# Kernel optimization log

Hardware: AMD Instinct MI355X
Metric: run time of the kernel (lower is better)

## Reference

```python
import jax, jax.numpy as jnp
import numpy as np

B, C, OUT, H, W, M1, M2, HID = 4, 64, 64, 256, 256, 32, 32, 64
COORD = C + 1  # MLP input: channels + 1 coordinate


def _lin(key, fan_in, fan_out):
    lim = 1.0 / np.sqrt(fan_in)
    kw, kb = jax.random.split(key)
    Wm = jax.random.uniform(kw, (fan_in, fan_out), minval=-lim, maxval=lim, dtype=jnp.float32)
    b = jax.random.uniform(kb, (fan_out,), minval=-lim, maxval=lim, dtype=jnp.float32)
    return Wm, b


def setup_inputs() -> dict:
    key = jax.random.key(0)
    ks = jax.random.split(key, 12)
    x = jax.random.normal(ks[0], (B, C, H, W), dtype=jnp.float32)
    # basis_w MLP: (C+1) -> HID -> HID -> 2*M2
    wW0, wb0 = _lin(ks[1], COORD, HID)
    wW1, wb1 = _lin(ks[2], HID, HID)
    wW2, wb2 = _lin(ks[3], HID, 2 * M2)
    # basis_h MLP: (C+1) -> HID -> HID -> 2*M1
    hW0, hb0 = _lin(ks[4], COORD, HID)
    hW1, hb1 = _lin(ks[5], HID, HID)
    hW2, hb2 = _lin(ks[6], HID, 2 * M1)
    std = (1.0 / (C + OUT)) ** 0.5
    Wf_re = std * jax.random.normal(ks[7], (C, OUT, M1, M2), dtype=jnp.float32)
    Wf_im = std * jax.random.normal(ks[8], (C, OUT, M1, M2), dtype=jnp.float32)
    mixer_w, mixer_b = _lin(ks[9], OUT, OUT)
    mixer_w = mixer_w.T  # (out, in) conv1x1 layout
    sc_w, sc_b = _lin(ks[10], C, OUT)
    sc_w = sc_w.T
    return {
        "x": x,
        "wW0": wW0, "wb0": wb0, "wW1": wW1, "wb1": wb1, "wW2": wW2, "wb2": wb2,
        "hW0": hW0, "hb0": hb0, "hW1": hW1, "hb1": hb1, "hW2": hW2, "hb2": hb2,
        "Wf_re": Wf_re, "Wf_im": Wf_im,
        "mixer_w": mixer_w, "mixer_b": mixer_b,
        "sc_w": sc_w, "sc_b": sc_b,
    }


def _gelu(v):
    return jax.nn.gelu(v, approximate=False)  # torch GELU is exact erf


def _cmlp(x, W0, b0, W1, b1, W2, b2, m):
    h = _gelu(x @ W0 + b0)
    h = _gelu(h @ W1 + b1)
    o = h @ W2 + b2
    return jax.lax.complex(o[..., :m], o[..., m:])


def reference(x, wW0, wb0, wW1, wb1, wW2, wb2,
              hW0, hb0, hW1, hb1, hW2, hb2,
              Wf_re, Wf_im, mixer_w, mixer_b, sc_w, sc_b):
    Bb, Cc, Hh, Ww = x.shape
    # --- W-direction basis: input is (values, w-coord) per pixel ---
    wc = jnp.linspace(-1.0, 1.0, Ww, dtype=jnp.float32)
    w_in = jnp.concatenate(
        [jnp.transpose(x, (0, 2, 3, 1)),
         jnp.broadcast_to(wc[None, None, :, None], (Bb, Hh, Ww, 1))], axis=-1)
    wb = _cmlp(w_in, wW0, wb0, wW1, wb1, wW2, wb2, M2)  # (B,H,W,m2) complex
    xc = x.astype(jnp.complex64)
    # separable transform along W: contract W against runtime basis
    tfw = jnp.einsum('bchw,bhwm->bchm', xc, wb)  # (B,C,H,m2)
    # --- H-direction basis: input is real part of W-transform + h-coord ---
    hcv = jnp.linspace(-1.0, 1.0, Hh, dtype=jnp.float32)
    h_in = jnp.concatenate(
        [jnp.transpose(tfw.real, (0, 3, 2, 1)),
         jnp.broadcast_to(hcv[None, None, :, None], (Bb, M2, Hh, 1))], axis=-1)
    hb = _cmlp(h_in, hW0, hb0, hW1, hb1, hW2, hb2, M1)  # (B,m2,H,m1) complex
    tfhw = jnp.einsum('bchm,bmhk->bckm', tfw, hb)  # (B,C,m1,m2)
    Wf = jax.lax.complex(Wf_re, Wf_im)  # (C_in, C_out, m1, m2)
    proc = jnp.einsum('bixy,oixy->boxy', tfhw, Wf)  # (B,out,m1,m2)
    # inverse transforms with conjugate-transposed bases
    rec = jnp.einsum('bokm,bmhk->bohm', proc, jnp.conj(hb))  # (B,out,H,m2)
    spatial = jnp.einsum('bohm,bhwm->bohw', rec, jnp.conj(wb)).real / (Hh * Ww)
    y = jnp.einsum('bchw,oc->bohw', spatial, mixer_w) + mixer_b[None, :, None, None]
    y = _gelu(y)
    y = y + jnp.einsum('bchw,oc->bohw', x, sc_w) + sc_b[None, :, None, None]
    return _gelu(y)
```

## Files before the change

### kernel.cpp

```cpp
#include <hip/hip_runtime.h>
#include <math.h>


typedef __attribute__((ext_vector_type(8))) short bf16x8;
typedef __attribute__((ext_vector_type(4))) float f32x4;

__device__ __forceinline__ float gelu_f(float v) {
    return 0.5f * v * (1.0f + erff(v * 0.70710678118654752440f));
}

__device__ __forceinline__ unsigned short f2b(float f) {
    union { float f; unsigned int u; } v; v.f = f;
    unsigned int u = v.u + 0x7FFFu + ((v.u >> 16) & 1u);
    return (unsigned short)(u >> 16);
}
__device__ __forceinline__ float b2f(unsigned short b) {
    union { unsigned int u; float f; } v; v.u = ((unsigned int)b) << 16;
    return v.f;
}

__global__ void k_prep(const float* __restrict__ wW0, const float* __restrict__ wW1,
                       const float* __restrict__ wW2,
                       const float* __restrict__ hW0, const float* __restrict__ hW1,
                       const float* __restrict__ hW2,
                       unsigned short* __restrict__ wT0, unsigned short* __restrict__ wT1,
                       unsigned short* __restrict__ wT2,
                       unsigned short* __restrict__ hT0, unsigned short* __restrict__ hT1,
                       unsigned short* __restrict__ hT2)
{
    const int t = threadIdx.x;
    for (int idx = t; idx < 64 * 96; idx += 256) {
        const int o = idx / 96, k = idx % 96;
        wT0[idx] = (k < 65) ? f2b(wW0[k * 64 + o]) : (unsigned short)0;
        hT0[idx] = (k < 65) ? f2b(hW0[k * 64 + o]) : (unsigned short)0;
    }
    for (int idx = t; idx < 4096; idx += 256) {
        const int o = idx >> 6, k = idx & 63;
        wT1[idx] = f2b(wW1[k * 64 + o]);
        wT2[idx] = f2b(wW2[k * 64 + o]);
        hT1[idx] = f2b(hW1[k * 64 + o]);
        hT2[idx] = f2b(hW2[k * 64 + o]);
    }
}

__global__ __launch_bounds__(256) void k_psum(const float* __restrict__ src,
                                              float* __restrict__ dst,
                                              int nparts, int part_stride)
{
    const int i = (blockIdx.x * 256 + threadIdx.x) * 4;
    float4 acc = *(const float4*)&src[i];
    for (int p = 1; p < nparts; ++p) {
        const float4 v = *(const float4*)&src[(size_t)p * part_stride + i];
        acc.x += v.x; acc.y += v.y; acc.z += v.z; acc.w += v.w;
    }
    *(float4*)&dst[i] = acc;
}

__global__ __launch_bounds__(256) void k_psum_procT(const float* __restrict__ src,
                                                    float* __restrict__ dst)
{
    const int idx = blockIdx.x * 256 + threadIdx.x;
    const int o = idx & 63, k = (idx >> 6) & 31, m = (idx >> 11) & 31, b = idx >> 16;
    const size_t in = (size_t)(b * 64 + o) * 1024 + k * 32 + m;
    const float re = src[in] + src[524288 + in];
    const float im = src[262144 + in] + src[524288 + 262144 + in];
    dst[idx] = re;
    dst[262144 + idx] = im;
}

constexpr int MLD = 104;

template<bool GELU, int NKC>
__device__ __forceinline__ void mfma_layer(
    const unsigned short* __restrict__ sW,
    const unsigned short* __restrict__ sAct,
    unsigned short* __restrict__ dst,
    const float* __restrict__ bias, int lane, int wv)
{
    const int arow = lane & 15;
    const int koff = (lane >> 4) * 8;
    const int crow = 16 * wv + (lane >> 4) * 4;
    const f32x4 zero = {0.f, 0.f, 0.f, 0.f};
    f32x4 acc[4] = {zero, zero, zero, zero};
#pragma unroll
    for (int kc = 0; kc < NKC; ++kc) {
        const bf16x8 a = *(const bf16x8*)&sW[(16 * wv + arow) * MLD + kc * 32 + koff];
#pragma unroll
        for (int nt = 0; nt < 4; ++nt) {
            const bf16x8 b = *(const bf16x8*)&sAct[(nt * 16 + arow) * MLD + kc * 32 + koff];
            acc[nt] = __builtin_amdgcn_mfma_f32_16x16x32_bf16(a, b, acc[nt], 0, 0, 0);
        }
    }
    const float4 bv = *(const float4*)&bias[crow];
#pragma unroll
    for (int nt = 0; nt < 4; ++nt) {
        const int px = nt * 16 + arow;
        float v0 = acc[nt][0] + bv.x;
        float v1 = acc[nt][1] + bv.y;
        float v2 = acc[nt][2] + bv.z;
        float v3 = acc[nt][3] + bv.w;
        if (GELU) { v0 = gelu_f(v0); v1 = gelu_f(v1); v2 = gelu_f(v2); v3 = gelu_f(v3); }
        ushort4 u;
        u.x = f2b(v0); u.y = f2b(v1); u.z = f2b(v2); u.w = f2b(v3);
        *(ushort4*)&dst[px * MLD + crow] = u;
    }
}

__device__ __forceinline__ void stage_wT96(const unsigned short* __restrict__ src,
                                           unsigned short* __restrict__ sW, int t) {
#pragma unroll
    for (int r = 0; r < 3; ++r) {
        const int idx = r * 256 + t;
        const int row = idx / 12, f = idx % 12;
        *(uint4*)&sW[row * MLD + f * 8] = *(const uint4*)&src[row * 96 + f * 8];
    }
}
__device__ __forceinline__ void stage_wT64(const unsigned short* __restrict__ src,
                                           unsigned short* __restrict__ sW, int t) {
#pragma unroll
    for (int r = 0; r < 2; ++r) {
        const int idx = r * 256 + t;
        const int row = idx >> 3, f = idx & 7;
        *(uint4*)&sW[row * MLD + f * 8] = *(const uint4*)&src[row * 64 + f * 8];
    }
}

__global__ __launch_bounds__(256) void k_wb_mlp2(
    const float* __restrict__ x,
    const unsigned short* __restrict__ wT0, const float* __restrict__ b0,
    const unsigned short* __restrict__ wT1, const float* __restrict__ b1,
    const unsigned short* __restrict__ wT2, const float* __restrict__ b2,
    unsigned short* __restrict__ wb_bf, unsigned short* __restrict__ wbT)
{
    __shared__ __align__(16) unsigned short sA[64 * MLD];
    __shared__ __align__(16) unsigned short sB[64 * MLD];
    __shared__ __align__(16) unsigned short sW[64 * MLD];
    const int blk = blockIdx.x;
    const int b = blk >> 10, h = (blk >> 2) & 255, wq = blk & 3;
    const int w0 = wq * 64;
    const int t = threadIdx.x;
    const int lane = t & 63, wv = t >> 6;

#pragma unroll
    for (int r = 0; r < 4; ++r) {
        const int idx = r * 256 + t;
        const int c = idx >> 4, wg = idx & 15;
        const float4 v = *(const float4*)&x[((size_t)(b * 64 + c) * 256 + h) * 256 + w0 + wg * 4];
        sA[(wg * 4 + 0) * MLD + c] = f2b(v.x);
        sA[(wg * 4 + 1) * MLD + c] = f2b(v.y);
        sA[(wg * 4 + 2) * MLD + c] = f2b(v.z);
        sA[(wg * 4 + 3) * MLD + c] = f2b(v.w);
    }
    if (t < 64) {
#pragma unroll
        for (int i = 1; i < 32; ++i) sA[t * MLD + 64 + i] = 0;
        sA[t * MLD + 64] = f2b((float)(w0 + t) * (2.0f / 255.0f) - 1.0f);
    }
    stage_wT96(wT0, sW, t);
    __syncthreads();
    mfma_layer<true, 3>(sW, sA, sB, b0, lane, wv);
    __syncthreads();
    stage_wT64(wT1, sW, t);
    __syncthreads();
    mfma_layer<true, 2>(sW, sB, sA, b1, lane, wv);
    __syncthreads();
    stage_wT64(wT2, sW, t);
    __syncthreads();
    mfma_layer<false, 2>(sW, sA, sB, b2, lane, wv);
    __syncthreads();

    const size_t pixbase = (size_t)(b * 256 + h) * 256 + w0;
#pragma unroll
    for (int r = 0; r < 2; ++r) {
        const int idx = r * 256 + t;
        const int px = idx >> 3, f = idx & 7;
        *(uint4*)&wb_bf[(pixbase + px) * 64 + f * 8] = *(const uint4*)&sB[px * MLD + f * 8];
    }
    const size_t tb2 = (size_t)(b * 256 + h) * 16384;
#pragma unroll
    for (int r = 0; r < 2; ++r) {
        const int idx = r * 256 + t;
        const int o = idx >> 3, g = idx & 7;
        unsigned short u[8];
#pragma unroll
        for (int j = 0; j < 8; ++j) u[j] = sB[(g * 8 + j) * MLD + o];
        *(uint4*)&wbT[tb2 + (size_t)o * 256 + w0 + g * 8] = *(uint4*)u;
    }
}

__global__ __launch_bounds__(256) void k_tfw2(
    const float* __restrict__ x,
    const unsigned short* __restrict__ wbT,
    float* __restrict__ tfwM)
{
    constexpr int TLD = 264;
    __shared__ __align__(16) unsigned short sW[64 * TLD];
    __shared__ __align__(16) unsigned short sX[64 * TLD];
    const int bh = blockIdx.x;
    const int b = bh >> 8, h = bh & 255;
    const int t = threadIdx.x;
    const int lane = t & 63, wv = t >> 6;

    const size_t wtb = (size_t)bh * 16384;
#pragma unroll
    for (int r = 0; r < 8; ++r) {
        const int idx = r * 256 + t;
        const int row = idx >> 5, f = idx & 31;
        *(uint4*)&sW[row * TLD + f * 8] = *(const uint4*)&wbT[wtb + (size_t)row * 256 + f * 8];
    }
#pragma unroll
    for (int r = 0; r < 16; ++r) {
        const int idx = r * 256 + t;
        const int c = idx >> 6, f = idx & 63;
        const float4 v = *(const float4*)&x[((size_t)(b * 64 + c) * 256 + h) * 256 + f * 4];
        ushort4 u; u.x = f2b(v.x); u.y = f2b(v.y); u.z = f2b(v.z); u.w = f2b(v.w);
        *(ushort4*)&sX[c * TLD + f * 4] = u;
    }
    __syncthreads();

    const int arow = lane & 15;
    const int koff = (lane >> 4) * 8;
    const f32x4 zero = {0.f, 0.f, 0.f, 0.f};
    f32x4 acc[4] = {zero, zero, zero, zero};
#pragma unroll
    for (int kc = 0; kc < 8; ++kc) {
        const bf16x8 a = *(const bf16x8*)&sW[(16 * wv + arow) * TLD + kc * 32 + koff];
#pragma unroll
        for (int nt = 0; nt < 4; ++nt) {
            const bf16x8 bb = *(const bf16x8*)&sX[(nt * 16 + arow) * TLD + kc * 32 + koff];
            acc[nt] = __builtin_amdgcn_mfma_f32_16x16x32_bf16(a, bb, acc[nt], 0, 0, 0);
        }
    }
    __syncthreads();
    float* sF = (float*)sW;
    const int crow = 16 * wv + (lane >> 4) * 4;
#pragma unroll
    for (int nt = 0; nt < 4; ++nt) {
        const int c = nt * 16 + arow;
#pragma unroll
        for (int j = 0; j < 4; ++j)
            sF[(crow + j) * 68 + c] = acc[nt][j];
    }
    __syncthreads();
#pragma unroll
    for (int r = 0; r < 4; ++r) {
        const int idx = r * 256 + t;
        const int m = idx >> 5, g = idx & 31;
        float4 v;
        v.x = sF[m * 68 + g * 2];
        v.y = sF[(m + 32) * 68 + g * 2];
        v.z = sF[m * 68 + g * 2 + 1];
        v.w = sF[(m + 32) * 68 + g * 2 + 1];
        *(float4*)&tfwM[((size_t)(b * 32 + m) * 256 + h) * 128 + g * 4] = v;
    }
}

__global__ __launch_bounds__(256) void k_hb_mlp2(
    const float* __restrict__ tfwM,
    const unsigned short* __restrict__ hT0, const float* __restrict__ b0,
    const unsigned short* __restrict__ hT1, const float* __restrict__ b1,
    const unsigned short* __restrict__ hT2, const float* __restrict__ b2,
    unsigned short* __restrict__ hb_bf)
{
    __shared__ __align__(16) unsigned short sA[64 * MLD];
    __shared__ __align__(16) unsigned short sB[64 * MLD];
    __shared__ __align__(16) unsigned short sW[64 * MLD];
    const int blk = blockIdx.x;
    const int bm = blk >> 2, hq = blk & 3;
    const int h0 = hq * 64;
    const int t = threadIdx.x;
    const int lane = t & 63, wv = t >> 6;

#pragma unroll
    for (int r = 0; r < 4; ++r) {
        const int idx = r * 256 + t;
        const int p = idx >> 4, f = idx & 15;
        const float* src = &tfwM[(size_t)(bm * 256 + h0 + p) * 128 + f * 8];
        const float4 u0 = *(const float4*)&src[0];
        const float4 u1 = *(const float4*)&src[4];
        ushort4 u;
        u.x = f2b(u0.x); u.y = f2b(u0.z); u.z = f2b(u1.x); u.w = f2b(u1.z);
        *(ushort4*)&sA[p * MLD + f * 4] = u;
    }
    if (t < 64) {
#pragma unroll
        for (int i = 1; i < 32; ++i) sA[t * MLD + 64 + i] = 0;
        sA[t * MLD + 64] = f2b((float)(h0 + t) * (2.0f / 255.0f) - 1.0f);
    }
    stage_wT96(hT0, sW, t);
    __syncthreads();
    mfma_layer<true, 3>(sW, sA, sB, b0, lane, wv);
    __syncthreads();
    stage_wT64(hT1, sW, t);
    __syncthreads();
    mfma_layer<true, 2>(sW, sB, sA, b1, lane, wv);
    __syncthreads();
    stage_wT64(hT2, sW, t);
    __syncthreads();
    mfma_layer<false, 2>(sW, sA, sB, b2, lane, wv);
    __syncthreads();

    const size_t pixbase = (size_t)bm * 256 + h0;
#pragma unroll
    for (int r = 0; r < 2; ++r) {
        const int idx = r * 256 + t;
        const int px = idx >> 3, f = idx & 7;
        *(uint4*)&hb_bf[(pixbase + px) * 64 + f * 8] = *(const uint4*)&sB[px * MLD + f * 8];
    }
}

__global__ __launch_bounds__(256) void k_tfhw3(
    const float* __restrict__ tfwM,
    const unsigned short* __restrict__ hb_bf,
    float* __restrict__ tfhw_p)
{
    __shared__ float hr[64 * 32];
    __shared__ float hi2[64 * 32];
    __shared__ float slab[32 * 64];
    const int blk = blockIdx.x;
    const int bm = blk >> 3, chalf = (blk >> 2) & 1, hq = blk & 3;
    const int b = bm >> 5, m = bm & 31;
    const int t = threadIdx.x;
#pragma unroll
    for (int r = 0; r < 2; ++r) {
        const int q = r * 256 + t;
        const int hl = q >> 3, f = q & 7;
        const uint4 raw = *(const uint4*)&hb_bf[((size_t)bm * 256 + hq * 64 + hl) * 64 + f * 8];
        const unsigned short* us = (const unsigned short*)&raw;
        float v[8];
#pragma unroll
        for (int j = 0; j < 8; ++j) v[j] = b2f(us[j]);
        float* dst = (f < 4) ? &hr[hl * 32 + f * 8] : &hi2[hl * 32 + (f - 4) * 8];
        float4 lo; lo.x = v[0]; lo.y = v[1]; lo.z = v[2]; lo.w = v[3];
        float4 hi; hi.x = v[4]; hi.y = v[5]; hi.z = v[6]; hi.w = v[7];
        *(float4*)&dst[0] = lo;
        *(float4*)&dst[4] = hi;
    }
    const int k = t & 31, cq = t >> 5;
    float accr[4] = {0.f, 0.f, 0.f, 0.f}, acci[4] = {0.f, 0.f, 0.f, 0.f};
    const size_t tbase = (size_t)bm * 32768;
    for (int ht = 0; ht < 2; ++ht) {
        __syncthreads();
#pragma unroll
        for (int r = 0; r < 2; ++r) {
            const int q = r * 256 + t;
            const int hl = q >> 3, f = q & 7;
            *(float4*)&slab[hl * 64 + f * 4] =
                *(const float4*)&tfwM[tbase + (size_t)(hq * 64 + ht * 32 + hl) * 128 + chalf * 64 + f * 4];
        }
        __syncthreads();
#pragma unroll 8
        for (int hl = 0; hl < 32; ++hl) {
            const float hrv = hr[(ht * 32 + hl) * 32 + k];
            const float hiv = hi2[(ht * 32 + hl) * 32 + k];
            const float4 u0 = *(const float4*)&slab[hl * 64 + cq * 8];
            const float4 u1 = *(const float4*)&slab[hl * 64 + cq * 8 + 4];
            accr[0] = fmaf(u0.x, hrv, fmaf(-u0.y, hiv, accr[0]));
            acci[0] = fmaf(u0.x, hiv, fmaf( u0.y, hrv, acci[0]));
            accr[1] = fmaf(u0.z, hrv, fmaf(-u0.w, hiv, accr[1]));
            acci[1] = fmaf(u0.z, hiv, fmaf( u0.w, hrv, acci[1]));
            accr[2] = fmaf(u1.x, hrv, fmaf(-u1.y, hiv, accr[2]));
            acci[2] = fmaf(u1.x, hiv, fmaf( u1.y, hrv, acci[2]));
            accr[3] = fmaf(u1.z, hrv, fmaf(-u1.w, hiv, accr[3]));
            acci[3] = fmaf(u1.z, hiv, fmaf( u1.w, hrv, acci[3]));
        }
    }
    float* tp = tfhw_p + (size_t)hq * 524288;
#pragma unroll
    for (int i = 0; i < 4; ++i) {
        const int c = chalf * 32 + cq * 4 + i;
        const size_t po = ((size_t)(b * 64 + c) * 32 + k) * 32 + m;
        tp[po] = accr[i];
        tp[262144 + po] = acci[i];
    }
}

__global__ __launch_bounds__(256) void k_proc2(
    const float* __restrict__ tfhw,
    const float* __restrict__ Wf_re, const float* __restrict__ Wf_im,
    float* __restrict__ proc_p)
{
    const int blk = blockIdx.x;
    const int o = blk >> 3, kq = (blk >> 1) & 3, chalf = blk & 1;
    const int t = threadIdx.x;
    const int mo = kq * 256 + t;
    const float* tre = tfhw;
    const float* tim = tfhw + 262144;
    float accr[4] = {0.f, 0.f, 0.f, 0.f}, acci[4] = {0.f, 0.f, 0.f, 0.f};
    for (int cc = 0; cc < 32; ++cc) {
        const int c = chalf * 32 + cc;
        const float wfr = Wf_re[(size_t)(c * 64 + o) * 1024 + mo];
        const float wfi = Wf_im[(size_t)(c * 64 + o) * 1024 + mo];
#pragma unroll
        for (int bb = 0; bb < 4; ++bb) {
            const float tr = tre[(size_t)(bb * 64 + c) * 1024 + mo];
            const float ti = tim[(size_t)(bb * 64 + c) * 1024 + mo];
            accr[bb] = fmaf(tr, wfr, fmaf(-ti, wfi, accr[bb]));
            acci[bb] = fmaf(tr, wfi, fmaf(ti, wfr, acci[bb]));
        }
    }
    float* pp = proc_p + (size_t)chalf * 524288;
#pragma unroll
    for (int bb = 0; bb < 4; ++bb) {
        pp[(size_t)(bb * 64 + o) * 1024 + mo] = accr[bb];
        pp[262144 + (size_t)(bb * 64 + o) * 1024 + mo] = acci[bb];
    }
}

__global__ __launch_bounds__(256) void k_rec4(
    const float* __restrict__ procT,
    const unsigned short* __restrict__ hb_bf,
    unsigned short* __restrict__ recO)
{
    __shared__ float lhr[32 * 32];
    __shared__ float lhi[32 * 32];
    const int blk = blockIdx.x;
    const int bm = blk >> 3, hq = blk & 7;
    const int b = bm >> 5, m = bm & 31;
    const int t = threadIdx.x;
    {
        const int hl = t >> 3, f = t & 7;
        const uint4 raw = *(const uint4*)&hb_bf[((size_t)bm * 256 + hq * 32 + hl) * 64 + f * 8];
        const unsigned short* us = (const unsigned short*)&raw;
        float v[8];
#pragma unroll
        for (int j = 0; j < 8; ++j) v[j] = b2f(us[j]);
        float* dst = (f < 4) ? &lhr[hl * 32 + f * 8] : &lhi[hl * 32 + (f - 4) * 8];
        float4 lo; lo.x = v[0]; lo.y = v[1]; lo.z = v[2]; lo.w = v[3];
        float4 hi; hi.x = v[4]; hi.y = v[5]; hi.z = v[6]; hi.w = v[7];
        *(float4*)&dst[0] = lo;
        *(float4*)&dst[4] = hi;
    }
    const int o = t & 63, hg = t >> 6;
    const float* pr = procT + (size_t)(b * 32 + m) * 2048 + o;
    const float* pi = pr + 262144;
    float Pr[32], Pi[32];
#pragma unroll
    for (int k = 0; k < 32; ++k) {
        Pr[k] = pr[k * 64];
        Pi[k] = pi[k * 64];
    }
    __syncthreads();
    for (int hh = 0; hh < 8; ++hh) {
        const int hl = hg * 8 + hh;
        float ar = 0.f, ai = 0.f;
#pragma unroll
        for (int k4 = 0; k4 < 8; ++k4) {
            const float4 hr4 = *(const float4*)&lhr[hl * 32 + k4 * 4];
            const float4 hi4 = *(const float4*)&lhi[hl * 32 + k4 * 4];
            ar = fmaf(Pr[k4*4+0], hr4.x, fmaf(Pi[k4*4+0], hi4.x, ar));
            ai = fmaf(Pi[k4*4+0], hr4.x, fmaf(-Pr[k4*4+0], hi4.x, ai));
            ar = fmaf(Pr[k4*4+1], hr4.y, fmaf(Pi[k4*4+1], hi4.y, ar));
            ai = fmaf(Pi[k4*4+1], hr4.y, fmaf(-Pr[k4*4+1], hi4.y, ai));
            ar = fmaf(Pr[k4*4+2], hr4.z, fmaf(Pi[k4*4+2], hi4.z, ar));
            ai = fmaf(Pi[k4*4+2], hr4.z, fmaf(-Pr[k4*4+2], hi4.z, ai));
            ar = fmaf(Pr[k4*4+3], hr4.w, fmaf(Pi[k4*4+3], hi4.w, ar));
            ai = fmaf(Pi[k4*4+3], hr4.w, fmaf(-Pr[k4*4+3], hi4.w, ai));
        }
        const int h = hq * 32 + hl;
        const size_t rb = ((size_t)(b * 256 + h) * 64 + o) * 64;
        recO[rb + m]      = f2b(ar);
        recO[rb + 32 + m] = f2b(ai);
    }
}

__global__ __launch_bounds__(256) void k_final4(
    const float* __restrict__ x,
    const unsigned short* __restrict__ wb_bf,
    const unsigned short* __restrict__ recO,
    const float* __restrict__ mw, const float* __restrict__ mb,
    const float* __restrict__ scw, const float* __restrict__ scb,
    float* __restrict__ out)
{
    constexpr int LD = 72;
    __shared__ __align__(16) unsigned short sWb[64 * LD];
    __shared__ __align__(16) unsigned short sR [64 * LD];
    __shared__ __align__(16) unsigned short sX [64 * LD];
    __shared__ __align__(16) unsigned short sS [64 * LD];
    const int blk = blockIdx.x;
    const int b = blk >> 10, h = (blk >> 2) & 255, wq = blk & 3;
    const int w0 = wq * 64;
    const int t = threadIdx.x;
    const int lane = t & 63, wv = t >> 6;
    const size_t pixbase = (size_t)(b * 256 + h) * 256 + w0;

#pragma unroll
    for (int r = 0; r < 2; ++r) {
        const int idx = r * 256 + t;
        const int px = idx >> 3, f = idx & 7;
        *(uint4*)&sWb[px * LD + f * 8] = *(const uint4*)&wb_bf[(pixbase + px) * 64 + f * 8];
    }
    const size_t recbase = (size_t)(b * 256 + h) * 4096;
#pragma unroll
    for (int r = 0; r < 2; ++r) {
        const int idx = r * 256 + t;
        const int o = idx >> 3, f = idx & 7;
        *(uint4*)&sR[o * LD + f * 8] = *(const uint4*)&recO[recbase + (size_t)o * 64 + f * 8];
    }
#pragma unroll
    for (int r = 0; r < 4; ++r) {
        const int idx = r * 256 + t;
        const int c = idx >> 4, wg = idx & 15;
        const float4 v = *(const float4*)&x[((size_t)(b * 64 + c) * 256 + h) * 256 + w0 + wg * 4];
        sX[(wg * 4 + 0) * LD + c] = f2b(v.x);
        sX[(wg * 4 + 1) * LD + c] = f2b(v.y);
        sX[(wg * 4 + 2) * LD + c] = f2b(v.z);
        sX[(wg * 4 + 3) * LD + c] = f2b(v.w);
    }
    __syncthreads();

    const int arow = lane & 15;
    const int koff = (lane >> 4) * 8;
    const f32x4 zero = {0.f, 0.f, 0.f, 0.f};

    f32x4 accA[4] = {zero, zero, zero, zero};
#pragma unroll
    for (int kc = 0; kc < 2; ++kc) {
        const bf16x8 a = *(const bf16x8*)&sR[(16 * wv + arow) * LD + kc * 32 + koff];
#pragma unroll
        for (int nt = 0; nt < 4; ++nt) {
            const bf16x8 bb = *(const bf16x8*)&sWb[(nt * 16 + arow) * LD + kc * 32 + koff];
            accA[nt] = __builtin_amdgcn_mfma_f32_16x16x32_bf16(a, bb, accA[nt], 0, 0, 0);
        }
    }
    __syncthreads();

    const int crow = 16 * wv + (lane >> 4) * 4;
#pragma unroll
    for (int nt = 0; nt < 4; ++nt) {
        const int px = nt * 16 + arow;
#pragma unroll
        for (int j = 0; j < 4; ++j)
            sS[px * LD + crow + j] = f2b(accA[nt][j] * (1.0f / 65536.0f));
    }
#pragma unroll
    for (int r = 0; r < 4; ++r) {
        const int idx = r * 256 + t;
        const int o = idx >> 4, cq = idx & 15;
        const float4 v1 = *(const float4*)&mw[o * 64 + cq * 4];
        ushort4 u1;
        u1.x = f2b(v1.x); u1.y = f2b(v1.y); u1.z = f2b(v1.z); u1.w = f2b(v1.w);
        *(ushort4*)&sWb[o * LD + cq * 4] = u1;
        const float4 v2 = *(const float4*)&scw[o * 64 + cq * 4];
        ushort4 u2;
        u2.x = f2b(v2.x); u2.y = f2b(v2.y); u2.z = f2b(v2.z); u2.w = f2b(v2.w);
        *(ushort4*)&sR[o * LD + cq * 4] = u2;
    }
    __syncthreads();

    f32x4 accB[4] = {zero, zero, zero, zero};
    f32x4 accC[4] = {zero, zero, zero, zero};
#pragma unroll
    for (int kc = 0; kc < 2; ++kc) {
        const bf16x8 am = *(const bf16x8*)&sWb[(16 * wv + arow) * LD + kc * 32 + koff];
        const bf16x8 as = *(const bf16x8*)&sR [(16 * wv + arow) * LD + kc * 32 + koff];
#pragma unroll
        for (int nt = 0; nt < 4; ++nt) {
            const bf16x8 bs = *(const bf16x8*)&sS[(nt * 16 + arow) * LD + kc * 32 + koff];
            const bf16x8 bx = *(const bf16x8*)&sX[(nt * 16 + arow) * LD + kc * 32 + koff];
            accB[nt] = __builtin_amdgcn_mfma_f32_16x16x32_bf16(am, bs, accB[nt], 0, 0, 0);
            accC[nt] = __builtin_amdgcn_mfma_f32_16x16x32_bf16(as, bx, accC[nt], 0, 0, 0);
        }
    }

#pragma unroll
    for (int nt = 0; nt < 4; ++nt) {
        const int px = nt * 16 + arow;
#pragma unroll
        for (int j = 0; j < 4; ++j) {
            const int o = crow + j;
            const float y = gelu_f(accB[nt][j] + mb[o]);
            const float z = y + accC[nt][j] + scb[o];
            out[((size_t)(b * 64 + o) * 256 + h) * 256 + w0 + px] = gelu_f(z);
        }
    }
}

extern "C" void kernel_launch(void* const* d_in, const int* in_sizes, int n_in,
                              void* d_out, int out_size, void* d_ws, size_t ws_size,
                              hipStream_t stream) {
    const float* x    = (const float*)d_in[0];
    const float* wW0  = (const float*)d_in[1];
    const float* wb0  = (const float*)d_in[2];
    const float* wW1  = (const float*)d_in[3];
    const float* wb1  = (const float*)d_in[4];
    const float* wW2  = (const float*)d_in[5];
    const float* wb2  = (const float*)d_in[6];
    const float* hW0  = (const float*)d_in[7];
    const float* hb0  = (const float*)d_in[8];
    const float* hW1  = (const float*)d_in[9];
    const float* hb1  = (const float*)d_in[10];
    const float* hW2  = (const float*)d_in[11];
    const float* hb2  = (const float*)d_in[12];
    const float* Wf_re = (const float*)d_in[13];
    const float* Wf_im = (const float*)d_in[14];
    const float* mw   = (const float*)d_in[15];
    const float* mbv  = (const float*)d_in[16];
    const float* scw  = (const float*)d_in[17];
    const float* scb  = (const float*)d_in[18];

    char* base = (char*)d_ws;
    unsigned short* wb_bf = (unsigned short*)(base + 0);
    unsigned short* wbT   = (unsigned short*)(base + 33554432);
    float* tfwM   = (float*)(base + 67108864);
    unsigned short* hb_bf = (unsigned short*)(base + 83886080);
    float* tfhw_p = (float*)(base + 88080384);
    float* tfhw   = (float*)(base + 96468992);
    float* proc_p = (float*)(base + 98566144);
    float* procT  = (float*)(base + 102760448);
    unsigned short* recO = (unsigned short*)(base + 104857600);
    unsigned short* wT0 = (unsigned short*)(base + 113246208);
    unsigned short* wT1 = (unsigned short*)(base + 113258496);
    unsigned short* wT2 = (unsigned short*)(base + 113266688);
    unsigned short* hT0 = (unsigned short*)(base + 113274880);
    unsigned short* hT1 = (unsigned short*)(base + 113287168);
    unsigned short* hT2 = (unsigned short*)(base + 113295360);

    k_prep<<<1, 256, 0, stream>>>(wW0, wW1, wW2, hW0, hW1, hW2,
                                  wT0, wT1, wT2, hT0, hT1, hT2);
    k_wb_mlp2<<<4096, 256, 0, stream>>>(x, wT0, wb0, wT1, wb1, wT2, wb2, wb_bf, wbT);
    k_tfw2<<<1024, 256, 0, stream>>>(x, wbT, tfwM);
    k_hb_mlp2<<<512, 256, 0, stream>>>(tfwM, hT0, hb0, hT1, hb1, hT2, hb2, hb_bf);
    k_tfhw3<<<1024, 256, 0, stream>>>(tfwM, hb_bf, tfhw_p);
    k_psum<<<1024, 256, 0, stream>>>(tfhw_p, tfhw, 4, 524288);
    k_proc2<<<512, 256, 0, stream>>>(tfhw, Wf_re, Wf_im, proc_p);
    k_psum_procT<<<1024, 256, 0, stream>>>(proc_p, procT);
    k_rec4<<<1024, 256, 0, stream>>>(procT, hb_bf, recO);
    k_final4<<<4096, 256, 0, stream>>>(x, wb_bf, recO, mw, mbv, scw, scb, (float*)d_out);
}
```

Baseline: 209.5 us.

## Replace erff with polynomial GELU, shuffle-transpose x staging, fuse wbT store

Replaces exact erff in GELU with an Abramowitz-Stegun polynomial using a hardware reciprocal and fast exp, aiming to cut the transcendental cost in the MLP and epilogue kernels. It adds a cross-lane shuffle transpose that stages x into LDS with 4-element vector writes instead of scalar 2-byte scatters. The zero padding is written with vector stores, and the last MLP layer writes bias-added outputs straight to the transposed global basis, dropping a separate LDS-transpose pass. The erf approximation has about 1e-7 absolute error, which adds a small accuracy change. The direct wbT writes are scattered 2-byte global stores and may coalesce poorly.

```diff
diff --git a/kernel.cpp b/kernel.cpp
--- a/kernel.cpp
+++ b/kernel.cpp
@@ -6,7 +6,18 @@
 typedef __attribute__((ext_vector_type(4))) float f32x4;
 
 __device__ __forceinline__ float gelu_f(float v) {
-    return 0.5f * v * (1.0f + erff(v * 0.70710678118654752440f));
+    const float u = v * 0.70710678118654752440f;
+    const float xa = fabsf(u);
+    const float t = __builtin_amdgcn_rcpf(fmaf(0.3275911f, xa, 1.0f));
+    float p = fmaf(1.061405429f, t, -1.453152027f);
+    p = fmaf(p, t, 1.421413741f);
+    p = fmaf(p, t, -0.284496736f);
+    p = fmaf(p, t, 0.254829592f);
+    p *= t;
+    const float e = __expf(-xa * xa);
+    float erfv = fmaf(-p, e, 1.0f);
+    erfv = (u < 0.0f) ? -erfv : erfv;
+    return 0.5f * v * (1.0f + erfv);
 }
 
 __device__ __forceinline__ unsigned short f2b(float f) {
@@ -17,6 +28,39 @@
 __device__ __forceinline__ float b2f(unsigned short b) {
     union { unsigned int u; float f; } v; v.u = ((unsigned int)b) << 16;
     return v.f;
+}
+
+__device__ __forceinline__ void stage_xT(const float* __restrict__ x,
+    unsigned short* __restrict__ sA, int b, int h, int w0, int t, int LD)
+{
+    const int lane = t & 63, wv = t >> 6;
+    const int g = lane >> 4, wg = lane & 15;
+#pragma unroll
+    for (int r = 0; r < 4; ++r) {
+        const int cb = r * 16 + wv * 4;
+        const float4 v = *(const float4*)&x[((size_t)(b * 64 + cb + g) * 256 + h) * 256 + w0 + wg * 4];
+        const float bx = __shfl_xor(v.x, 16);
+        const float by = __shfl_xor(v.y, 16);
+        const float bz = __shfl_xor(v.z, 16);
+        const float bw = __shfl_xor(v.w, 16);
+        float4 s1;
+        s1.x = ((g & 1) == 0) ? v.x : by;
+        s1.y = ((g & 1) == 0) ? bx  : v.y;
+        s1.z = ((g & 1) == 0) ? v.z : bw;
+        s1.w = ((g & 1) == 0) ? bz  : v.w;
+        const float cx = __shfl_xor(s1.x, 32);
+        const float cy = __shfl_xor(s1.y, 32);
+        const float cz = __shfl_xor(s1.z, 32);
+        const float cw = __shfl_xor(s1.w, 32);
+        float4 s2;
+        s2.x = ((g & 2) == 0) ? s1.x : cz;
+        s2.y = ((g & 2) == 0) ? s1.y : cw;
+        s2.z = ((g & 2) == 0) ? cx   : s1.z;
+        s2.w = ((g & 2) == 0) ? cy   : s1.w;
+        ushort4 u;
+        u.x = f2b(s2.x); u.y = f2b(s2.y); u.z = f2b(s2.z); u.w = f2b(s2.w);
+        *(ushort4*)&sA[(wg * 4 + g) * LD + cb] = u;
+    }
 }
 
 __global__ void k_prep(const float* __restrict__ wW0, const float* __restrict__ wW1,
@@ -141,19 +185,13 @@
     const int t = threadIdx.x;
     const int lane = t & 63, wv = t >> 6;
 
-#pragma unroll
-    for (int r = 0; r < 4; ++r) {
-        const int idx = r * 256 + t;
-        const int c = idx >> 4, wg = idx & 15;
-        const float4 v = *(const float4*)&x[((size_t)(b * 64 + c) * 256 + h) * 256 + w0 + wg * 4];
-        sA[(wg * 4 + 0) * MLD + c] = f2b(v.x);
-        sA[(wg * 4 + 1) * MLD + c] = f2b(v.y);
-        sA[(wg * 4 + 2) * MLD + c] = f2b(v.z);
-        sA[(wg * 4 + 3) * MLD + c] = f2b(v.w);
-    }
+    stage_xT(x, sA, b, h, w0, t, MLD);
     if (t < 64) {
-#pragma unroll
-        for (int i = 1; i < 32; ++i) sA[t * MLD + 64 + i] = 0;
+        const uint4 z = {0, 0, 0, 0};
+        *(uint4*)&sA[t * MLD + 64] = z;
+        *(uint4*)&sA[t * MLD + 72] = z;
+        *(uint4*)&sA[t * MLD + 80] = z;
+        *(uint4*)&sA[t * MLD + 88] = z;
         sA[t * MLD + 64] = f2b((float)(w0 + t) * (2.0f / 255.0f) - 1.0f);
     }
     stage_wT96(wT0, sW, t);
@@ -166,7 +204,38 @@
     __syncthreads();
     stage_wT64(wT2, sW, t);
     __syncthreads();
-    mfma_layer<false, 2>(sW, sA, sB, b2, lane, wv);
+    {
+        const int arow = lane & 15;
+        const int koff = (lane >> 4) * 8;
+        const int crow = 16 * wv + (lane >> 4) * 4;
+        const f32x4 zero = {0.f, 0.f, 0.f, 0.f};
+        f32x4 acc[4] = {zero, zero, zero, zero};
+#pragma unroll
+        for (int kc = 0; kc < 2; ++kc) {
+            const bf16x8 a = *(const bf16x8*)&sW[(16 * wv + arow) * MLD + kc * 32 + koff];
+#pragma unroll
+            for (int nt = 0; nt < 4; ++nt) {
+                const bf16x8 bb = *(const bf16x8*)&sA[(nt * 16 + arow) * MLD + kc * 32 + koff];
+                acc[nt] = __builtin_amdgcn_mfma_f32_16x16x32_bf16(a, bb, acc[nt], 0, 0, 0);
+            }
+        }
+        const float4 bv = *(const float4*)&b2[crow];
+        const size_t tb2 = (size_t)(b * 256 + h) * 16384;
+#pragma unroll
+        for (int nt = 0; nt < 4; ++nt) {
+            const int px = nt * 16 + arow;
+            ushort4 u;
+            u.x = f2b(acc[nt][0] + bv.x);
+            u.y = f2b(acc[nt][1] + bv.y);
+            u.z = f2b(acc[nt][2] + bv.z);
+            u.w = f2b(acc[nt][3] + bv.w);
+            *(ushort4*)&sB[px * MLD + crow] = u;
+            wbT[tb2 + (size_t)(crow + 0) * 256 + w0 + px] = u.x;
+            wbT[tb2 + (size_t)(crow + 1) * 256 + w0 + px] = u.y;
+            wbT[tb2 + (size_t)(crow + 2) * 256 + w0 + px] = u.z;
+            wbT[tb2 + (size_t)(crow + 3) * 256 + w0 + px] = u.w;
+        }
+    }
     __syncthreads();
 
     const size_t pixbase = (size_t)(b * 256 + h) * 256 + w0;
@@ -175,16 +244,6 @@
         const int idx = r * 256 + t;
         const int px = idx >> 3, f = idx & 7;
         *(uint4*)&wb_bf[(pixbase + px) * 64 + f * 8] = *(const uint4*)&sB[px * MLD + f * 8];
-    }
-    const size_t tb2 = (size_t)(b * 256 + h) * 16384;
-#pragma unroll
-    for (int r = 0; r < 2; ++r) {
-        const int idx = r * 256 + t;
-        const int o = idx >> 3, g = idx & 7;
-        unsigned short u[8];
-#pragma unroll
-        for (int j = 0; j < 8; ++j) u[j] = sB[(g * 8 + j) * MLD + o];
-        *(uint4*)&wbT[tb2 + (size_t)o * 256 + w0 + g * 8] = *(uint4*)u;
     }
 }
 
@@ -283,8 +342,11 @@
         *(ushort4*)&sA[p * MLD + f * 4] = u;
     }
     if (t < 64) {
-#pragma unroll
-        for (int i = 1; i < 32; ++i) sA[t * MLD + 64 + i] = 0;
+        const uint4 z = {0, 0, 0, 0};
+        *(uint4*)&sA[t * MLD + 64] = z;
+        *(uint4*)&sA[t * MLD + 72] = z;
+        *(uint4*)&sA[t * MLD + 80] = z;
+        *(uint4*)&sA[t * MLD + 88] = z;
         sA[t * MLD + 64] = f2b((float)(h0 + t) * (2.0f / 255.0f) - 1.0f);
     }
     stage_wT96(hT0, sW, t);
@@ -497,16 +559,7 @@
         const int o = idx >> 3, f = idx & 7;
         *(uint4*)&sR[o * LD + f * 8] = *(const uint4*)&recO[recbase + (size_t)o * 64 + f * 8];
     }
-#pragma unroll
-    for (int r = 0; r < 4; ++r) {
-        const int idx = r * 256 + t;
-        const int c = idx >> 4, wg = idx & 15;
-        const float4 v = *(const float4*)&x[((size_t)(b * 64 + c) * 256 + h) * 256 + w0 + wg * 4];
-        sX[(wg * 4 + 0) * LD + c] = f2b(v.x);
-        sX[(wg * 4 + 1) * LD + c] = f2b(v.y);
-        sX[(wg * 4 + 2) * LD + c] = f2b(v.z);
-        sX[(wg * 4 + 3) * LD + c] = f2b(v.w);
-    }
+    stage_xT(x, sX, b, h, w0, t, LD);
     __syncthreads();
 
     const int arow = lane & 15;
```

Measured after the change: 195.5 us. 6.7% less time.
